# Optimization experiments

Measured on AMD Instinct MI355X. Metric: run time of the kernel, lower is better.

The kernel has to match this reference:

```python
import jax, jax.numpy as jnp
import numpy as np

IN_DIM = 256
QK_DIM = IN_DIM // 8  # 32
NCLS = 19
B, H, W = 2, 64, 64


def conv3x3(x, w, b):
    # x: [B,C,H,W], w: [O,I,3,3] -> SAME padding, stride 1 (= pad=1 in torch)
    y = jax.lax.conv_general_dilated(x, w, (1, 1), 'SAME',
                                     dimension_numbers=('NCHW', 'OIHW', 'NCHW'))
    return y + b[None, :, None, None]


def setup_inputs() -> dict:
    key = jax.random.key(0)
    ks = jax.random.split(key, 20)
    s = 0.05
    inp = {
        'x': jax.random.normal(ks[0], (B, IN_DIM, H, W), jnp.float32),
        'modal_mask': jax.random.uniform(ks[1], (B, NCLS, H, W), jnp.float32),
        'amodal_mask': jax.random.uniform(ks[2], (B, NCLS, H, W), jnp.float32),
        'w_mp': jax.random.normal(ks[3], (NCLS, IN_DIM, 3, 3), jnp.float32) * s,
        'b_mp': jnp.zeros((NCLS,), jnp.float32),
        'w_ap': jax.random.normal(ks[4], (NCLS, IN_DIM, 3, 3), jnp.float32) * s,
        'b_ap': jnp.zeros((NCLS,), jnp.float32),
        'w_q': jax.random.normal(ks[5], (QK_DIM, IN_DIM + NCLS, 3, 3), jnp.float32) * s,
        'b_q': jnp.zeros((QK_DIM,), jnp.float32),
        'w_k': jax.random.normal(ks[6], (QK_DIM, IN_DIM + NCLS, 3, 3), jnp.float32) * s,
        'b_k': jnp.zeros((QK_DIM,), jnp.float32),
        'w_v': jax.random.normal(ks[7], (IN_DIM, IN_DIM, 3, 3), jnp.float32) * s,
        'b_v': jnp.zeros((IN_DIM,), jnp.float32),
        'w_comp': jax.random.normal(ks[8], (IN_DIM, IN_DIM + 2 * NCLS, 3, 3), jnp.float32) * s,
        'b_comp': jnp.zeros((IN_DIM,), jnp.float32),
        'w_out': jax.random.normal(ks[9], (IN_DIM, 3 * IN_DIM, 3, 3), jnp.float32) * s,
        'b_out': jnp.zeros((IN_DIM,), jnp.float32),
        # SELayer(in_dim, reduction=8): Linear(c, c//8, bias=False), Linear(c//8, c, bias=False)
        'w_se1': jax.random.normal(ks[10], (IN_DIM // 8, IN_DIM), jnp.float32) * s,
        'w_se2': jax.random.normal(ks[11], (IN_DIM, IN_DIM // 8), jnp.float32) * s,
    }
    return inp


def reference(x, modal_mask, amodal_mask, w_mp, b_mp, w_ap, b_ap, w_q, b_q,
              w_k, b_k, w_v, b_v, w_comp, b_comp, w_out, b_out, w_se1, w_se2):
    b, c, h, w = x.shape
    n = h * w
    # masks already at (h, w): nearest interpolate is identity
    modal_x = conv3x3(x, w_mp, b_mp) * modal_mask
    amodal_x = conv3x3(x, w_ap, b_ap) * amodal_mask
    inp = jnp.concatenate([x, modal_x, amodal_x], axis=1)
    out = conv3x3(inp, w_comp, b_comp)
    # SE layer
    y = out.mean(axis=(2, 3))                                # [b, c]
    y = jax.nn.sigmoid(jax.nn.relu(y @ w_se1.T) @ w_se2.T)   # [b, c]
    out_a = out * y[:, :, None, None]
    # dual-softmax spatial attention
    q = conv3x3(jnp.concatenate([x, modal_mask], axis=1), w_q, b_q).reshape(b, QK_DIM, n)
    k = conv3x3(jnp.concatenate([x, amodal_mask], axis=1), w_k, b_k).reshape(b, QK_DIM, n)
    v = conv3x3(x, w_v, b_v).reshape(b, c, n)
    energy = jnp.einsum('bdn,bdm->bnm', q, k)                # [b, n, n]
    attn = jax.nn.softmax(energy, axis=-1)                   # softmax over keys
    attn_t = jax.nn.softmax(energy, axis=1)                  # softmax over queries (of E^T rows)
    # out_b = bmm(v, attn^T); out_c = bmm(v, softmax(E^T,-1)^T)
    out_b = jnp.einsum('bcn,bmn->bcm', v, attn).reshape(b, c, h, w)
    out_c = jnp.einsum('bcn,bnm->bcm', v, attn_t).reshape(b, c, h, w)
    out = jnp.concatenate([out_a, out_b, out_c], axis=1)
    return conv3x3(out, w_out, b_out)
```

## Files before the change

kernel.cpp:

```cpp
#include <hip/hip_runtime.h>
#include <math.h>

#define HW 4096
#define IMG 64
#define PIX66 (66 * 66)

typedef short short8 __attribute__((ext_vector_type(8)));
typedef float f32x4 __attribute__((ext_vector_type(4)));

__device__ __forceinline__ unsigned short f2bf(float f) {
    unsigned int u = __float_as_uint(f);
    u += 0x7fff + ((u >> 16) & 1);
    return (unsigned short)(u >> 16);
}
__device__ __forceinline__ float bf2f(unsigned short h) {
    return __uint_as_float(((unsigned int)h) << 16);
}
__device__ __forceinline__ unsigned int pkbf(float a, float b) {
    unsigned int ua = __float_as_uint(a) + 0x8000u;
    unsigned int ub = __float_as_uint(b) + 0x8000u;
    return __builtin_amdgcn_perm(ub, ua, 0x07060302u);
}

__device__ __forceinline__ void gll16(const unsigned short* g, unsigned short* l) {
    __builtin_amdgcn_global_load_lds(
        (const __attribute__((address_space(1))) unsigned int*)(g),
        (__attribute__((address_space(3))) unsigned int*)(l), 16, 0, 0);
}

__device__ __forceinline__ int pxor(int pix) { return (pix ^ (pix >> 2)) & 3; }
__device__ __forceinline__ int p32o(int pix, int c) {
    return pix * 32 + ((((c >> 3) ^ pxor(pix)) & 3) << 3) + (c & 7);
}

struct WtJob {
    const float* w;
    unsigned short* dh;
    unsigned short* dl;
    int OC, OCpad, C0, K0pad, C1, Ktot;
};

__global__ __launch_bounds__(256) void k_wt_all(WtJob J0, WtJob J1, WtJob J2,
                                                WtJob J3, WtJob J4, WtJob J5,
                                                WtJob J6) {
    WtJob J;
    switch (blockIdx.y) {
        case 0: J = J0; break;
        case 1: J = J1; break;
        case 2: J = J2; break;
        case 3: J = J3; break;
        case 4: J = J4; break;
        case 5: J = J5; break;
        default: J = J6; break;
    }
    int idx = blockIdx.x * 256 + threadIdx.x;
    int KS = J.Ktot >> 5;
    int n = 9 * KS * J.OCpad * 32;
    if (idx >= n) return;
    int kk = idx & 31;
    int rest = idx >> 5;
    int oc = rest % J.OCpad;
    rest /= J.OCpad;
    int kg = rest % KS;
    int tap = rest / KS;
    int k = kg * 32 + kk;
    float v = 0.f;
    if (oc < J.OC) {
        int ic = -1;
        if (k < J.C0) ic = k;
        else if (k >= J.K0pad && (k - J.K0pad) < J.C1) ic = J.C0 + (k - J.K0pad);
        if (ic >= 0) v = J.w[((size_t)oc * (J.C0 + J.C1) + ic) * 9 + tap];
    }
    unsigned short hi = f2bf(v);
    J.dh[idx] = hi;
    if (J.dl) J.dl[idx] = f2bf(v - bf2f(hi));
}

__global__ __launch_bounds__(256) void k_build_x(const float* __restrict__ x,
                                                 unsigned short* __restrict__ xh,
                                                 unsigned short* __restrict__ xl,
                                                 unsigned short* __restrict__ ipad) {
    int b = blockIdx.z, c0 = blockIdx.y * 64, p0 = blockIdx.x * 64;
    __shared__ float s[64][65];
    int t = threadIdx.x;
    for (int i = t; i < 4096; i += 256) {
        int c = i >> 6, p = i & 63;
        s[p][c] = x[((size_t)b * 256 + c0 + c) * HW + p0 + p];
    }
    __syncthreads();
    for (int i = t; i < 4096; i += 256) {
        int c = i & 63, p = i >> 6;
        float f = s[p][c];
        unsigned short hi = f2bf(f);
        unsigned short lo = f2bf(f - bf2f(hi));
        int pp = p0 + p;
        int y = pp >> 6, xx = pp & 63;
        int pix = (y + 1) * 66 + xx + 1;
        int C = c0 + c;
        size_t ix = (size_t)(b * 8 + (C >> 5)) * (PIX66 * 32) + p32o(pix, C & 31);
        xh[ix] = hi;
        xl[ix] = lo;
        ipad[(size_t)(b * 10 + (C >> 5)) * (PIX66 * 32) + p32o(pix, C & 31)] = hi;
    }
}

__global__ __launch_bounds__(256) void k_build_mask2(
    const float* __restrict__ m0, const float* __restrict__ m1,
    unsigned short* __restrict__ d0h, unsigned short* __restrict__ d0l,
    unsigned short* __restrict__ d1h, unsigned short* __restrict__ d1l) {
    const float* m = blockIdx.y ? m1 : m0;
    unsigned short* dh = blockIdx.y ? d1h : d0h;
    unsigned short* dl = blockIdx.y ? d1l : d0l;
    int idx = blockIdx.x * 256 + threadIdx.x;
    int c = idx & 31;
    int p = (idx >> 5) & 4095;
    int b = idx >> 17;
    float f = (c < 19) ? m[((size_t)b * 19 + c) * HW + p] : 0.f;
    unsigned short hi = f2bf(f);
    int y = p >> 6, xx = p & 63;
    int pix = (y + 1) * 66 + xx + 1;
    dh[(size_t)b * (PIX66 * 32) + p32o(pix, c)] = hi;
    dl[(size_t)b * (PIX66 * 32) + p32o(pix, c)] = f2bf(f - bf2f(hi));
}

struct DJob {
    const unsigned short* s1h;
    const unsigned short* s1l;
    const unsigned short* wth;
    const unsigned short* wtl;
    const float* bias;
    unsigned short* d1;
    unsigned short* d2;
    const float* mask;
    int chBase;
    int mode;
    int split;
    int KS1;
};

__global__ __launch_bounds__(128, 2) void conv_direct_all(
    const unsigned short* __restrict__ s0h, const unsigned short* __restrict__ s0l,
    DJob j0, DJob j1, DJob j2, DJob j3) {
    DJob J;
    switch (blockIdx.y) {
        case 0: J = j0; break;
        case 1: J = j1; break;
        case 2: J = j2; break;
        default: J = j3; break;
    }
    const int KS0 = 8;
    int KS = KS0 + J.KS1;
    int ST = 9 * KS;
    int b = blockIdx.z;
    int t = threadIdx.x, w = t >> 6, l = t & 63, quad = l >> 4, ln = l & 15;
    int pBase = blockIdx.x * 64 + w * 32;

    int padpix[2];
#pragma unroll
    for (int tn = 0; tn < 2; ++tn) {
        int p = pBase + tn * 16 + ln;
        padpix[tn] = ((p >> 6) + 1) * 66 + (p & 63) + 1;
    }
    size_t aoff[2];
#pragma unroll
    for (int tm = 0; tm < 2; ++tm) aoff[tm] = (size_t)(tm * 16 + ln) * 32 + quad * 8;

    const unsigned short* S0H = s0h + (size_t)b * KS0 * PIX66 * 32;
    const unsigned short* S0L = s0l + (size_t)b * KS0 * PIX66 * 32;
    const unsigned short* S1H = J.KS1 ? J.s1h + (size_t)b * PIX66 * 32
                                      : (const unsigned short*)0;
    const unsigned short* S1L = J.KS1 ? J.s1l + (size_t)b * PIX66 * 32
                                      : (const unsigned short*)0;

    f32x4 acc[2][2];
#pragma unroll
    for (int i = 0; i < 2; ++i)
#pragma unroll
        for (int j = 0; j < 2; ++j) acc[i][j] = (f32x4){0.f, 0.f, 0.f, 0.f};

    int tap = 0, kg = 0;
    auto adv = [&]() { if (++kg == KS) { kg = 0; ++tap; } };
    auto loadStep = [&](int ltap, int lkg, short8* bh, short8* bl, short8* ah,
                        short8* al) {
        int d3 = ltap / 3;
        int dpix = (d3 - 1) * 66 + (ltap - d3 * 3 - 1);
        const unsigned short* SpH;
        const unsigned short* SpL;
        long plane;
        if (lkg < KS0) {
            SpH = S0H; SpL = S0L; plane = (long)lkg * PIX66 * 32;
        } else {
            SpH = S1H; SpL = S1L; plane = 0;
        }
#pragma unroll
        for (int tn = 0; tn < 2; ++tn) {
            int pix2 = padpix[tn] + dpix;
            long off = plane + (long)pix2 * 32 + (((quad ^ pxor(pix2)) & 3) << 3);
            bh[tn] = *(const short8*)(SpH + off);
            if (J.split) bl[tn] = *(const short8*)(SpL + off);
        }
        const unsigned short* WTh = J.wth + (size_t)(ltap * KS + lkg) * 32 * 32;
        ah[0] = *(const short8*)(WTh + aoff[0]);
        ah[1] = *(const short8*)(WTh + aoff[1]);
        if (J.split) {
            const unsigned short* WTl = J.wtl + (size_t)(ltap * KS + lkg) * 32 * 32;
            al[0] = *(const short8*)(WTl + aoff[0]);
            al[1] = *(const short8*)(WTl + aoff[1]);
        }
    };

    short8 BH[2][2], AH[2][2], BL[2][2], AL[2][2];
#pragma unroll
    for (int u = 0; u < 2; ++u) { loadStep(tap, kg, BH[u], BL[u], AH[u], AL[u]); adv(); }

    for (int s = 0; s < ST; s += 2) {
#pragma unroll
        for (int u = 0; u < 2; ++u) {
            if (s + u < ST) {
#pragma unroll
                for (int tm = 0; tm < 2; ++tm)
#pragma unroll
                    for (int tn = 0; tn < 2; ++tn) {
                        acc[tm][tn] = __builtin_amdgcn_mfma_f32_16x16x32_bf16(
                            AH[u][tm], BH[u][tn], acc[tm][tn], 0, 0, 0);
                        if (J.split) {
                            acc[tm][tn] = __builtin_amdgcn_mfma_f32_16x16x32_bf16(
                                AL[u][tm], BH[u][tn], acc[tm][tn], 0, 0, 0);
                            acc[tm][tn] = __builtin_amdgcn_mfma_f32_16x16x32_bf16(
                                AH[u][tm], BL[u][tn], acc[tm][tn], 0, 0, 0);
                        }
                    }
                if (s + u + 2 < ST) { loadStep(tap, kg, BH[u], BL[u], AH[u], AL[u]); adv(); }
            }
        }
    }

#pragma unroll
    for (int tm = 0; tm < 2; ++tm) {
#pragma unroll
        for (int r = 0; r < 4; ++r) {
            int oc = tm * 16 + quad * 4 + r;
#pragma unroll
            for (int tn = 0; tn < 2; ++tn) {
                int p = pBase + tn * 16 + ln;
                if (J.mode == 1) {
                    if (oc < 19) {
                        float v = (acc[tm][tn][r] + J.bias[oc]) *
                                  J.mask[((size_t)b * 19 + oc) * HW + p];
                        int ch = J.chBase + oc;
                        J.d1[(size_t)(b * 10 + (ch >> 5)) * (PIX66 * 32) +
                             p32o(padpix[tn], ch & 31)] = f2bf(v);
                    }
                } else {
                    float v = acc[tm][tn][r] + J.bias[oc];
                    unsigned short hi = f2bf(v);
                    J.d1[((size_t)b * HW + p) * 32 + oc] = hi;
                    J.d2[((size_t)b * HW + p) * 32 + oc] = f2bf(v - bf2f(hi));
                }
            }
        }
    }
}

struct LJob {
    const unsigned short* src;
    const unsigned short* wt;
    unsigned short* dstb16;
    int KS;
    int nseg;
    int doSum;
};

__global__ __launch_bounds__(128, 3) void conv_lds(LJob j0, LJob j1, int ocgPerJob,
                                                   float* __restrict__ ybuf) {
    int jy = blockIdx.y;
    LJob J = (jy >= ocgPerJob) ? j1 : j0;
    int ocBase = ((jy >= ocgPerJob) ? jy - ocgPerJob : jy) * 64;
    int z = blockIdx.z;
    int b = z & 1, seg = z >> 1;
    int kgPer = J.KS / J.nseg;
    int kgBeg = seg * kgPer, kgEnd = kgBeg + kgPer;
    int ry = blockIdx.x * 2;
    int t = threadIdx.x, w = t >> 6, l = t & 63, quad = l >> 4, ln = l & 15;

    __shared__ unsigned short sB[2][264 * 32];

    const unsigned short* S = J.src + (size_t)b * J.KS * PIX66 * 32;
    const size_t bStageBase = (size_t)(ry * 66) * 32;

    f32x4 acc[4][4];
#pragma unroll
    for (int i = 0; i < 4; ++i)
#pragma unroll
        for (int j = 0; j < 4; ++j) acc[i][j] = (f32x4){0.f, 0.f, 0.f, 0.f};

    {
        const unsigned short* gB = S + (size_t)kgBeg * PIX66 * 32 + bStageBase;
        for (int i = t; i < 1056; i += 128) gll16(gB + (size_t)i * 8, sB[0] + (size_t)i * 8);
    }

    for (int kg = kgBeg; kg < kgEnd; ++kg) {
        int cur = (kg - kgBeg) & 1;
        __syncthreads();
        if (kg + 1 < kgEnd) {
            const unsigned short* gB = S + (size_t)(kg + 1) * PIX66 * 32 + bStageBase;
            for (int i = t; i < 1056; i += 128)
                gll16(gB + (size_t)i * 8, sB[cur ^ 1] + (size_t)i * 8);
        }
        const unsigned short* sBc = sB[cur];
#pragma unroll
        for (int tap = 0; tap < 9; ++tap) {
            const unsigned short* gA =
                J.wt + ((size_t)(tap * J.KS + kg) * 256 + ocBase) * 32;
            int dy = tap / 3 - 1, dx = tap % 3 - 1;
            int lpBase = (1 + w + dy) * 66 + 1 + dx;
            short8 bf[4], af[4];
#pragma unroll
            for (int tn = 0; tn < 4; ++tn) {
                int lp = lpBase + tn * 16 + ln;
                int P = ry * 66 + lp;
                bf[tn] = *(const short8*)(sBc + (size_t)lp * 32 +
                                          (((quad ^ pxor(P)) & 3) << 3));
            }
#pragma unroll
            for (int tm = 0; tm < 4; ++tm)
                af[tm] = *(const short8*)(gA + (size_t)(tm * 16 + ln) * 32 + quad * 8);
#pragma unroll
            for (int tm = 0; tm < 4; ++tm)
#pragma unroll
                for (int tn = 0; tn < 4; ++tn)
                    acc[tm][tn] = __builtin_amdgcn_mfma_f32_16x16x32_bf16(
                        af[tm], bf[tn], acc[tm][tn], 0, 0, 0);
        }
    }

    int prow = ry + w;
#pragma unroll
    for (int tm = 0; tm < 4; ++tm) {
#pragma unroll
        for (int r = 0; r < 4; ++r) {
            int oc = ocBase + tm * 16 + quad * 4 + r;
            float msum = 0.f;
#pragma unroll
            for (int tn = 0; tn < 4; ++tn) {
                int px = tn * 16 + ln;
                J.dstb16[((size_t)z * 256 + oc) * HW + prow * 64 + px] =
                    f2bf(acc[tm][tn][r]);
                msum += acc[tm][tn][r];
            }
            if (J.doSum) {
#pragma unroll
                for (int off = 8; off; off >>= 1) msum += __shfl_down(msum, off, 16);
                if (ln == 0) atomicAdd(&ybuf[b * 256 + oc], msum);
            }
        }
    }
}

__global__ __launch_bounds__(256) void vc_combine(
    const unsigned short* __restrict__ pV, const float* __restrict__ bv,
    unsigned short* __restrict__ vt,
    const unsigned short* __restrict__ pC, const float* __restrict__ bc,
    const float* __restrict__ sc, unsigned short* __restrict__ catN) {
    int idx = blockIdx.x * 256 + threadIdx.x;
    int p = idx & 4095;
    int oc = (idx >> 12) & 255;
    int b = idx >> 20;
    int prow = p >> 6, px = p & 63;
    float v = bf2f(pV[((size_t)b * 256 + oc) * HW + p]) +
              bf2f(pV[((size_t)(2 + b) * 256 + oc) * HW + p]) + bv[oc];
    int jc = ((px >> 3) ^ (oc & 7)) & 7;
    vt[(((size_t)b * 64 + prow) * 256 + oc) * 64 + jc * 8 + (px & 7)] = f2bf(v);
    float c = (bf2f(pC[((size_t)b * 256 + oc) * HW + p]) +
               bf2f(pC[((size_t)(2 + b) * 256 + oc) * HW + p]) + bc[oc]) *
              sc[b * 256 + oc];
    int pix = (prow + 1) * 66 + px + 1;
    catN[(size_t)(b * 24 + (oc >> 5)) * (PIX66 * 32) + p32o(pix, oc & 31)] = f2bf(c);
}

__global__ __launch_bounds__(256) void out_combine(const unsigned short* __restrict__ part,
                                                   const float* __restrict__ bias,
                                                   float* __restrict__ outp) {
    int idx = blockIdx.x * 256 + threadIdx.x;
    int p = idx & 4095;
    int oc = (idx >> 12) & 255;
    int b = idx >> 20;
    float v = bf2f(part[((size_t)(0 + b) * 256 + oc) * HW + p]) +
              bf2f(part[((size_t)(2 + b) * 256 + oc) * HW + p]) +
              bf2f(part[((size_t)(4 + b) * 256 + oc) * HW + p]) +
              bf2f(part[((size_t)(6 + b) * 256 + oc) * HW + p]) + bias[oc];
    outp[((size_t)b * 256 + oc) * HW + p] = v;
}

__global__ __launch_bounds__(512, 4) void flash_attn(
    const unsigned short* __restrict__ qt_h, const unsigned short* __restrict__ qt_l,
    const unsigned short* __restrict__ kt_h, const unsigned short* __restrict__ kt_l,
    const unsigned short* __restrict__ vt,
    unsigned short* __restrict__ pO, float* __restrict__ pm, float* __restrict__ pl) {
    int seg = blockIdx.y >> 1, mode = blockIdx.y & 1, b = blockIdx.z;
    size_t qkoff = (size_t)b * HW * 32;
    const unsigned short* Qh = (mode ? kt_h : qt_h) + qkoff;
    const unsigned short* Ql = (mode ? kt_l : qt_l) + qkoff;
    const unsigned short* Kh = (mode ? qt_h : kt_h) + qkoff;
    const unsigned short* Kl = (mode ? qt_l : kt_l) + qkoff;
    const unsigned short* Vt = vt + (size_t)b * 64 * 256 * 64;

    int t = threadIdx.x, w = t >> 6, l = t & 63, quad = l >> 4, ln = l & 15;
    int pg = w & 1, ch = w >> 1;
    int p0 = blockIdx.x * 64, pw = pg * 32;
    int cb = ch * 64;
    bool soft = (ch == (pg ? 3 : 0));

    __shared__ unsigned short sV[256 * 64];
    __shared__ unsigned short sP[64 * 68];
    __shared__ float sAl[64];

    short8 qbh[2], qbl[2];
    if (soft) {
#pragma unroll
        for (int pn = 0; pn < 2; ++pn) {
            size_t off = (size_t)(p0 + pw + pn * 16 + ln) * 32 + quad * 8;
            qbh[pn] = *(const short8*)(Qh + off);
            qbl[pn] = *(const short8*)(Ql + off);
        }
    }

    float m_run[2] = {-3.0e38f, -3.0e38f};
    float l_run[2] = {0.f, 0.f};
    f32x4 accO[4][2];
#pragma unroll
    for (int cs = 0; cs < 4; ++cs)
#pragma unroll
        for (int pn = 0; pn < 2; ++pn) accO[cs][pn] = (f32x4){0.f, 0.f, 0.f, 0.f};

    int jbBeg = seg * (HW / 2);
    for (int jb = jbBeg; jb < jbBeg + HW / 2; jb += 64) {
        __syncthreads();
        {
            const unsigned short* gV = Vt + (size_t)(jb >> 6) * (256 * 64);
#pragma unroll
            for (int i = 0; i < 4; ++i)
                gll16(gV + (size_t)(t + 512 * i) * 8, sV + (size_t)(t + 512 * i) * 8);
        }
        if (soft) {
            f32x4 sacc[2][4];
#pragma unroll
            for (int pn = 0; pn < 2; ++pn)
#pragma unroll
                for (int jj = 0; jj < 4; ++jj) sacc[pn][jj] = (f32x4){0.f, 0.f, 0.f, 0.f};
#pragma unroll
            for (int jj = 0; jj < 4; ++jj) {
                size_t off = (size_t)(jb + 16 * jj + ln) * 32 + quad * 8;
                short8 kh = *(const short8*)(Kh + off);
                short8 kr = *(const short8*)(Kl + off);
#pragma unroll
                for (int pn = 0; pn < 2; ++pn) {
                    sacc[pn][jj] = __builtin_amdgcn_mfma_f32_16x16x32_bf16(
                        kh, qbh[pn], sacc[pn][jj], 0, 0, 0);
                    sacc[pn][jj] = __builtin_amdgcn_mfma_f32_16x16x32_bf16(
                        kh, qbl[pn], sacc[pn][jj], 0, 0, 0);
                    sacc[pn][jj] = __builtin_amdgcn_mfma_f32_16x16x32_bf16(
                        kr, qbh[pn], sacc[pn][jj], 0, 0, 0);
                }
            }
#pragma unroll
            for (int pn = 0; pn < 2; ++pn) {
                float tmx = -3.0e38f;
#pragma unroll
                for (int jj = 0; jj < 4; ++jj)
#pragma unroll
                    for (int r = 0; r < 4; ++r) tmx = fmaxf(tmx, sacc[pn][jj][r]);
                tmx = fmaxf(tmx, __shfl_xor(tmx, 16));
                tmx = fmaxf(tmx, __shfl_xor(tmx, 32));
                float mnew = fmaxf(m_run[pn], tmx);
                float alpha = __expf(m_run[pn] - mnew);
                m_run[pn] = mnew;
                float psum = 0.f;
#pragma unroll
                for (int jj = 0; jj < 4; ++jj) {
                    float e0 = __expf(sacc[pn][jj][0] - mnew);
                    float e1 = __expf(sacc[pn][jj][1] - mnew);
                    float e2 = __expf(sacc[pn][jj][2] - mnew);
                    float e3 = __expf(sacc[pn][jj][3] - mnew);
                    psum += (e0 + e1) + (e2 + e3);
                    uint2 pk;
                    pk.x = pkbf(e0, e1);
                    pk.y = pkbf(e2, e3);
                    *(uint2*)(sP + (size_t)(pw + pn * 16 + ln) * 68 + jj * 16 +
                              quad * 4) = pk;
                }
                psum += __shfl_xor(psum, 16);
                psum += __shfl_xor(psum, 32);
                l_run[pn] = l_run[pn] * alpha + psum;
                if (quad == 0) sAl[pw + pn * 16 + ln] = alpha;
            }
        }
        __syncthreads();
        float al0 = sAl[pw + ln];
        float al1 = sAl[pw + 16 + ln];
#pragma unroll
        for (int cs = 0; cs < 4; ++cs) { accO[cs][0] *= al0; accO[cs][1] *= al1; }
#pragma unroll
        for (int j2 = 0; j2 < 2; ++j2) {
            short8 pb0 = *(const short8*)(sP + (size_t)(pw + ln) * 68 + j2 * 32 +
                                          quad * 8);
            short8 pb1 = *(const short8*)(sP + (size_t)(pw + 16 + ln) * 68 + j2 * 32 +
                                          quad * 8);
#pragma unroll
            for (int cs = 0; cs < 4; ++cs) {
                int c = cb + cs * 16 + ln;
                short8 va = *(const short8*)(
                    sV + (size_t)c * 64 + ((((j2 * 4 + quad) ^ (c & 7)) & 7) << 3));
                accO[cs][0] = __builtin_amdgcn_mfma_f32_16x16x32_bf16(
                    va, pb0, accO[cs][0], 0, 0, 0);
                accO[cs][1] = __builtin_amdgcn_mfma_f32_16x16x32_bf16(
                    va, pb1, accO[cs][1], 0, 0, 0);
            }
        }
    }

    int idx4 = (seg * 2 + mode) * 2 + b;
#pragma unroll
    for (int pn = 0; pn < 2; ++pn) {
        int p = p0 + pw + pn * 16 + ln;
        if (soft && quad == 0) {
            pm[(size_t)idx4 * HW + p] = m_run[pn];
            pl[(size_t)idx4 * HW + p] = l_run[pn];
        }
#pragma unroll
        for (int cs = 0; cs < 4; ++cs)
#pragma unroll
            for (int r = 0; r < 4; ++r) {
                int c = cb + cs * 16 + quad * 4 + r;
                pO[((size_t)idx4 * 256 + c) * HW + p] = f2bf(accO[cs][pn][r]);
            }
    }
}

__global__ __launch_bounds__(256) void attn_combine(const unsigned short* __restrict__ pO,
                                                    const float* __restrict__ pm,
                                                    const float* __restrict__ pl,
                                                    unsigned short* __restrict__ catN) {
    int b = blockIdx.z, mode = blockIdx.y;
    int t = threadIdx.x;
    int p = blockIdx.x * 64 + (t & 63);
    int c0 = (t >> 6) * 64;
    int i0 = mode * 2 + b;
    int i1 = 4 + mode * 2 + b;
    float m0 = pm[(size_t)i0 * HW + p], m1 = pm[(size_t)i1 * HW + p];
    float l0 = pl[(size_t)i0 * HW + p], l1 = pl[(size_t)i1 * HW + p];
    float M = fmaxf(m0, m1);
    float e0 = __expf(m0 - M), e1 = __expf(m1 - M);
    float inv = 1.f / (l0 * e0 + l1 * e1);
    e0 *= inv;
    e1 *= inv;
    int y = p >> 6, x = p & 63;
    int pix = (y + 1) * 66 + x + 1;
    for (int c = c0; c < c0 + 64; ++c) {
        float v = bf2f(pO[((size_t)i0 * 256 + c) * HW + p]) * e0 +
                  bf2f(pO[((size_t)i1 * 256 + c) * HW + p]) * e1;
        int cf = 256 + mode * 256 + c;
        catN[(size_t)(b * 24 + (cf >> 5)) * (PIX66 * 32) + p32o(pix, cf & 31)] = f2bf(v);
    }
}

__global__ __launch_bounds__(256) void se_mlp_kernel(const float* __restrict__ y,
                                                     const float* __restrict__ bcomp,
                                                     const float* __restrict__ w1,
                                                     const float* __restrict__ w2,
                                                     float* __restrict__ sc) {
    int b = blockIdx.x, t = threadIdx.x;
    __shared__ float sy[256], sh[32];
    sy[t] = y[b * 256 + t] * (1.f / 4096.f) + bcomp[t];
    __syncthreads();
    if (t < 32) {
        float s = 0.f;
        for (int c = 0; c < 256; ++c) s = fmaf(w1[t * 256 + c], sy[c], s);
        sh[t] = fmaxf(s, 0.f);
    }
    __syncthreads();
    float s = 0.f;
#pragma unroll
    for (int h = 0; h < 32; ++h) s = fmaf(w2[t * 32 + h], sh[h], s);
    sc[b * 256 + t] = 1.f / (1.f + __expf(-s));
}

extern "C" void kernel_launch(void* const* d_in, const int* in_sizes, int n_in,
                              void* d_out, int out_size, void* d_ws, size_t ws_size,
                              hipStream_t stream) {
    const float* x      = (const float*)d_in[0];
    const float* mmask  = (const float*)d_in[1];
    const float* amask  = (const float*)d_in[2];
    const float* w_mp   = (const float*)d_in[3];
    const float* b_mp   = (const float*)d_in[4];
    const float* w_ap   = (const float*)d_in[5];
    const float* b_ap   = (const float*)d_in[6];
    const float* w_q    = (const float*)d_in[7];
    const float* b_q    = (const float*)d_in[8];
    const float* w_k    = (const float*)d_in[9];
    const float* b_k    = (const float*)d_in[10];
    const float* w_v    = (const float*)d_in[11];
    const float* b_v    = (const float*)d_in[12];
    const float* w_comp = (const float*)d_in[13];
    const float* b_comp = (const float*)d_in[14];
    const float* w_out  = (const float*)d_in[15];
    const float* b_out  = (const float*)d_in[16];
    const float* w_se1  = (const float*)d_in[17];
    const float* w_se2  = (const float*)d_in[18];

    unsigned short* us = (unsigned short*)d_ws;
    size_t o = 0;
    unsigned short* xpad_hi = us + o; o += (size_t)2 * 8 * PIX66 * 32;
    unsigned short* xpad_lo = us + o; o += (size_t)2 * 8 * PIX66 * 32;
    unsigned short* mq_hi   = us + o; o += (size_t)2 * PIX66 * 32;
    unsigned short* mq_lo   = us + o; o += (size_t)2 * PIX66 * 32;
    unsigned short* ma_hi   = us + o; o += (size_t)2 * PIX66 * 32;
    unsigned short* ma_lo   = us + o; o += (size_t)2 * PIX66 * 32;
    unsigned short* ipad    = us + o; o += (size_t)2 * 10 * PIX66 * 32;
    unsigned short* catN    = us + o; o += (size_t)2 * 24 * PIX66 * 32;
    size_t zeroBytes = o * sizeof(unsigned short);
    unsigned short* wt_mp = us + o; o += (size_t)9 * 8 * 32 * 32;
    unsigned short* wt_ap = us + o; o += (size_t)9 * 8 * 32 * 32;
    unsigned short* wt_qh = us + o; o += (size_t)9 * 9 * 32 * 32;
    unsigned short* wt_ql = us + o; o += (size_t)9 * 9 * 32 * 32;
    unsigned short* wt_kh = us + o; o += (size_t)9 * 9 * 32 * 32;
    unsigned short* wt_kl = us + o; o += (size_t)9 * 9 * 32 * 32;
    unsigned short* wt_v  = us + o; o += (size_t)9 * 8 * 256 * 32;
    unsigned short* wt_cp = us + o; o += (size_t)9 * 10 * 256 * 32;
    unsigned short* wt_ot = us + o; o += (size_t)9 * 24 * 256 * 32;
    unsigned short* qt_h  = us + o; o += (size_t)2 * HW * 32;
    unsigned short* qt_l  = us + o; o += (size_t)2 * HW * 32;
    unsigned short* kt_h  = us + o; o += (size_t)2 * HW * 32;
    unsigned short* kt_l  = us + o; o += (size_t)2 * HW * 32;
    unsigned short* vt    = us + o; o += (size_t)2 * 64 * 256 * 64;
    unsigned short* pV16  = us + o; o += (size_t)4 * 256 * HW;
    unsigned short* pC16  = us + o; o += (size_t)4 * 256 * HW;
    unsigned short* pA16  = us + o; o += (size_t)8 * 256 * HW;
    unsigned short* pO16  = us + o; o += (size_t)8 * 256 * HW;
    float* fp = (float*)(us + o);
    size_t fo = 0;
    float* pmb  = fp + fo; fo += (size_t)8 * HW;
    float* plb  = fp + fo; fo += (size_t)8 * HW;
    float* ybuf = fp + fo; fo += 512;
    float* sbuf = fp + fo; fo += 512;
    size_t need = o * sizeof(unsigned short) + fo * sizeof(float);
    if (ws_size < need) return;

    float* outp = (float*)d_out;

    hipMemsetAsync(us, 0, zeroBytes, stream);
    hipMemsetAsync(ybuf, 0, 512 * sizeof(float), stream);

    WtJob W0{w_mp,   wt_mp, (unsigned short*)0, 19, 32, 256, 256, 0, 256};
    WtJob W1{w_ap,   wt_ap, (unsigned short*)0, 19, 32, 256, 256, 0, 256};
    WtJob W2{w_q,    wt_qh, wt_ql,             32, 32, 256, 256, 19, 288};
    WtJob W3{w_k,    wt_kh, wt_kl,             32, 32, 256, 256, 19, 288};
    WtJob W4{w_v,    wt_v,  (unsigned short*)0, 256, 256, 256, 256, 0, 256};
    WtJob W5{w_comp, wt_cp, (unsigned short*)0, 256, 256, 294, 320, 0, 320};
    WtJob W6{w_out,  wt_ot, (unsigned short*)0, 256, 256, 768, 768, 0, 768};
    k_wt_all<<<dim3((9 * 24 * 256 * 32 + 255) / 256, 7), 256, 0, stream>>>(
        W0, W1, W2, W3, W4, W5, W6);

    k_build_x<<<dim3(64, 4, 2), 256, 0, stream>>>(x, xpad_hi, xpad_lo, ipad);
    k_build_mask2<<<dim3(1024, 2), 256, 0, stream>>>(mmask, amask, mq_hi, mq_lo,
                                                     ma_hi, ma_lo);

    const unsigned short* NUS = (const unsigned short*)0;
    unsigned short* NUSo = (unsigned short*)0;
    float* NF = (float*)0;

    DJob dm{NUS, NUS, wt_mp, NUS, b_mp, ipad, NUSo, mmask, 256, 1, 0, 0};
    DJob da{NUS, NUS, wt_ap, NUS, b_ap, ipad, NUSo, amask, 275, 1, 0, 0};
    DJob dq{mq_hi, mq_lo, wt_qh, wt_ql, b_q, qt_h, qt_l, NF, 0, 2, 1, 1};
    DJob dk{ma_hi, ma_lo, wt_kh, wt_kl, b_k, kt_h, kt_l, NF, 0, 2, 1, 1};
    conv_direct_all<<<dim3(64, 4, 2), 128, 0, stream>>>(xpad_hi, xpad_lo, dm, da, dq, dk);

    LJob lv{xpad_hi, wt_v, pV16, 8, 2, 0};
    LJob lc{ipad, wt_cp, pC16, 10, 2, 1};
    conv_lds<<<dim3(32, 8, 4), 128, 0, stream>>>(lv, lc, 4, ybuf);

    se_mlp_kernel<<<2, 256, 0, stream>>>(ybuf, b_comp, w_se1, w_se2, sbuf);
    vc_combine<<<8192, 256, 0, stream>>>(pV16, b_v, vt, pC16, b_comp, sbuf, catN);

    flash_attn<<<dim3(64, 4, 2), 512, 0, stream>>>(qt_h, qt_l, kt_h, kt_l, vt,
                                                   pA16, pmb, plb);
    attn_combine<<<dim3(64, 2, 2), 256, 0, stream>>>(pA16, pmb, plb, catN);

    LJob lo{catN, wt_ot, pO16, 24, 4, 0};
    conv_lds<<<dim3(32, 4, 8), 128, 0, stream>>>(lo, lo, 4, NF);
    out_combine<<<8192, 256, 0, stream>>>(pO16, b_out, outp);
}
```

Measured before the change: 416.5 us.

## Drop split-K for V and comp convs and fuse epilogues into conv_lds

```diff
diff --git a/kernel.cpp b/kernel.cpp
--- a/kernel.cpp
+++ b/kernel.cpp
@@ -266,9 +266,10 @@
     const unsigned short* src;
     const unsigned short* wt;
     unsigned short* dstb16;
+    const float* bias;
     int KS;
     int nseg;
-    int doSum;
+    int mode;
 };
 
 __global__ __launch_bounds__(128, 3) void conv_lds(LJob j0, LJob j1, int ocgPerJob,
@@ -277,9 +278,18 @@
     LJob J = (jy >= ocgPerJob) ? j1 : j0;
     int ocBase = ((jy >= ocgPerJob) ? jy - ocgPerJob : jy) * 64;
     int z = blockIdx.z;
-    int b = z & 1, seg = z >> 1;
-    int kgPer = J.KS / J.nseg;
-    int kgBeg = seg * kgPer, kgEnd = kgBeg + kgPer;
+    int b, kgBeg, kgEnd;
+    if (J.mode == 0) {
+        b = z & 1;
+        int seg = z >> 1;
+        int kgPer = J.KS / J.nseg;
+        kgBeg = seg * kgPer;
+        kgEnd = kgBeg + kgPer;
+    } else {
+        b = z;
+        kgBeg = 0;
+        kgEnd = J.KS;
+    }
     int ry = blockIdx.x * 2;
     int t = threadIdx.x, w = t >> 6, l = t & 63, quad = l >> 4, ln = l & 15;
 
@@ -344,38 +354,29 @@
 #pragma unroll
             for (int tn = 0; tn < 4; ++tn) {
                 int px = tn * 16 + ln;
-                J.dstb16[((size_t)z * 256 + oc) * HW + prow * 64 + px] =
-                    f2bf(acc[tm][tn][r]);
-                msum += acc[tm][tn][r];
-            }
-            if (J.doSum) {
+                if (J.mode == 0) {
+                    J.dstb16[((size_t)z * 256 + oc) * HW + prow * 64 + px] =
+                        f2bf(acc[tm][tn][r]);
+                } else if (J.mode == 1) {
+                    float v = acc[tm][tn][r] + J.bias[oc];
+                    int jc = ((px >> 3) ^ (oc & 7)) & 7;
+                    J.dstb16[(((size_t)b * 64 + prow) * 256 + oc) * 64 + jc * 8 +
+                             (px & 7)] = f2bf(v);
+                } else {
+                    float v = acc[tm][tn][r] + J.bias[oc];
+                    int pix = (prow + 1) * 66 + px + 1;
+                    J.dstb16[(size_t)(b * 24 + (oc >> 5)) * (PIX66 * 32) +
+                             p32o(pix, oc & 31)] = f2bf(v);
+                    msum += acc[tm][tn][r];
+                }
+            }
+            if (J.mode == 2) {
 #pragma unroll
                 for (int off = 8; off; off >>= 1) msum += __shfl_down(msum, off, 16);
                 if (ln == 0) atomicAdd(&ybuf[b * 256 + oc], msum);
             }
         }
     }
-}
-
-__global__ __launch_bounds__(256) void vc_combine(
-    const unsigned short* __restrict__ pV, const float* __restrict__ bv,
-    unsigned short* __restrict__ vt,
-    const unsigned short* __restrict__ pC, const float* __restrict__ bc,
-    const float* __restrict__ sc, unsigned short* __restrict__ catN) {
-    int idx = blockIdx.x * 256 + threadIdx.x;
-    int p = idx & 4095;
-    int oc = (idx >> 12) & 255;
-    int b = idx >> 20;
-    int prow = p >> 6, px = p & 63;
-    float v = bf2f(pV[((size_t)b * 256 + oc) * HW + p]) +
-              bf2f(pV[((size_t)(2 + b) * 256 + oc) * HW + p]) + bv[oc];
-    int jc = ((px >> 3) ^ (oc & 7)) & 7;
-    vt[(((size_t)b * 64 + prow) * 256 + oc) * 64 + jc * 8 + (px & 7)] = f2bf(v);
-    float c = (bf2f(pC[((size_t)b * 256 + oc) * HW + p]) +
-               bf2f(pC[((size_t)(2 + b) * 256 + oc) * HW + p]) + bc[oc]) *
-              sc[b * 256 + oc];
-    int pix = (prow + 1) * 66 + px + 1;
-    catN[(size_t)(b * 24 + (oc >> 5)) * (PIX66 * 32) + p32o(pix, oc & 31)] = f2bf(c);
 }
 
 __global__ __launch_bounds__(256) void out_combine(const unsigned short* __restrict__ part,
@@ -583,6 +584,19 @@
 #pragma unroll
     for (int h = 0; h < 32; ++h) s = fmaf(w2[t * 32 + h], sh[h], s);
     sc[b * 256 + t] = 1.f / (1.f + __expf(-s));
+}
+
+__global__ __launch_bounds__(256) void se_scale_cat(unsigned short* __restrict__ catN,
+                                                    const float* __restrict__ sc) {
+    int idx = blockIdx.x * 256 + threadIdx.x;
+    int c = idx & 255;
+    int p = (idx >> 8) & 4095;
+    int b = idx >> 20;
+    int y = p >> 6, x = p & 63;
+    int pix = (y + 1) * 66 + x + 1;
+    unsigned short* q =
+        catN + (size_t)(b * 24 + (c >> 5)) * (PIX66 * 32) + p32o(pix, c & 31);
+    *q = f2bf(bf2f(*q) * sc[b * 256 + c]);
 }
 
 extern "C" void kernel_launch(void* const* d_in, const int* in_sizes, int n_in,
@@ -633,8 +647,6 @@
     unsigned short* kt_h  = us + o; o += (size_t)2 * HW * 32;
     unsigned short* kt_l  = us + o; o += (size_t)2 * HW * 32;
     unsigned short* vt    = us + o; o += (size_t)2 * 64 * 256 * 64;
-    unsigned short* pV16  = us + o; o += (size_t)4 * 256 * HW;
-    unsigned short* pC16  = us + o; o += (size_t)4 * 256 * HW;
     unsigned short* pA16  = us + o; o += (size_t)8 * 256 * HW;
     unsigned short* pO16  = us + o; o += (size_t)8 * 256 * HW;
     float* fp = (float*)(us + o);
@@ -675,18 +687,18 @@
     DJob dk{ma_hi, ma_lo, wt_kh, wt_kl, b_k, kt_h, kt_l, NF, 0, 2, 1, 1};
     conv_direct_all<<<dim3(64, 4, 2), 128, 0, stream>>>(xpad_hi, xpad_lo, dm, da, dq, dk);
 
-    LJob lv{xpad_hi, wt_v, pV16, 8, 2, 0};
-    LJob lc{ipad, wt_cp, pC16, 10, 2, 1};
-    conv_lds<<<dim3(32, 8, 4), 128, 0, stream>>>(lv, lc, 4, ybuf);
+    LJob lv{xpad_hi, wt_v, vt, b_v, 8, 1, 1};
+    LJob lc{ipad, wt_cp, catN, b_comp, 10, 1, 2};
+    conv_lds<<<dim3(32, 8, 2), 128, 0, stream>>>(lv, lc, 4, ybuf);
 
     se_mlp_kernel<<<2, 256, 0, stream>>>(ybuf, b_comp, w_se1, w_se2, sbuf);
-    vc_combine<<<8192, 256, 0, stream>>>(pV16, b_v, vt, pC16, b_comp, sbuf, catN);
+    se_scale_cat<<<8192, 256, 0, stream>>>(catN, sbuf);
 
     flash_attn<<<dim3(64, 4, 2), 512, 0, stream>>>(qt_h, qt_l, kt_h, kt_l, vt,
                                                    pA16, pmb, plb);
     attn_combine<<<dim3(64, 2, 2), 256, 0, stream>>>(pA16, pmb, plb, catN);
 
-    LJob lo{catN, wt_ot, pO16, 24, 4, 0};
-    conv_lds<<<dim3(32, 4, 8), 128, 0, stream>>>(lo, lo, 4, NF);
+    LJob lo{catN, wt_ot, pO16, NF, 24, 4, 0};
+    conv_lds<<<dim3(32, 4, 8), 128, 0, stream>>>(lo, lo, 4, ybuf);
     out_combine<<<8192, 256, 0, stream>>>(pO16, b_out, outp);
 }
```

After: 444.6 us. +6.8%, slower.
